# Kernel tuning notes

Measured on AMD Instinct MI355X. Metric: run time of the kernel, lower is better.

The kernel has to match this reference:

```python
import jax, jax.numpy as jnp
import numpy as np

B, T, D, HD, HN, O = 32, 512, 512, 64, 16, 512
EPS = 1e-5


def setup_inputs() -> dict:
    key = jax.random.key(0)
    ks = jax.random.split(key, 12)
    s = lambda fan_in: 1.0 / np.sqrt(fan_in)
    inp = {
        "inputs": jax.random.normal(ks[0], (B, T, D), dtype=jnp.float32),
        "Wq": jax.random.uniform(ks[1], (HN, D, HD), jnp.float32, -s(D), s(D)),
        "bq": jnp.zeros((HN, HD), jnp.float32),
        "Wk": jax.random.uniform(ks[2], (HN, D, HD), jnp.float32, -s(D), s(D)),
        "bk": jnp.zeros((HN, HD), jnp.float32),
        "Wv": jax.random.uniform(ks[3], (HN, D, HD), jnp.float32, -s(D), s(D)),
        "bv": jnp.zeros((HN, HD), jnp.float32),
        "Wr": jax.random.uniform(ks[4], (D, O), jnp.float32, -s(D), s(D)),
        "br": jnp.zeros((O,), jnp.float32),
        "Wo": jax.random.uniform(ks[5], (HN * HD, O), jnp.float32, -s(HN * HD), s(HN * HD)),
        "bo": jnp.zeros((O,), jnp.float32),
        "ln1_w": jnp.ones((O,), jnp.float32),
        "ln1_b": jnp.zeros((O,), jnp.float32),
        "Wfc": jax.random.uniform(ks[6], (O, O), jnp.float32, -s(O), s(O)),
        "bfc": jnp.zeros((O,), jnp.float32),
        "ln2_w": jnp.ones((O,), jnp.float32),
        "ln2_b": jnp.zeros((O,), jnp.float32),
    }
    return inp


def _layernorm(x, w, b):
    mu = jnp.mean(x, axis=-1, keepdims=True)
    var = jnp.mean(jnp.square(x - mu), axis=-1, keepdims=True)
    return (x - mu) * jax.lax.rsqrt(var + EPS) * w + b


def reference(inputs, Wq, bq, Wk, bk, Wv, bv, Wr, br, Wo, bo,
              ln1_w, ln1_b, Wfc, bfc, ln2_w, ln2_b):
    # causal mask: multiply-then-subtract as in the original
    score_mask = jnp.tril(jnp.ones((T, T), jnp.float32))        # [T,T]
    padding_mask = (score_mask == 0).astype(jnp.float32) * 1e9  # [T,T]

    residual = inputs @ Wr + br                                  # [B,T,O]

    # batched per-head projections with nonstandard activations
    q = jax.nn.relu(jnp.einsum('btd,hdf->bhtf', inputs, Wq) + bq[None, :, None, :])
    k = jax.nn.relu(jnp.einsum('btd,hdf->bhtf', inputs, Wk) + bk[None, :, None, :])
    v = jnp.tanh(jnp.einsum('btd,hdf->bhtf', inputs, Wv) + bv[None, :, None, :])

    scores = jnp.einsum('bhtf,bhsf->bhts', q, k) / jnp.sqrt(jnp.float32(HD))
    scores = scores * score_mask - padding_mask                  # [B,H,T,T]
    weights = jax.nn.softmax(scores, axis=-1)
    heads = jnp.einsum('bhts,bhsf->bhtf', weights, v)            # [B,H,T,HD]

    # concat heads (head order preserved) + tanh output projection
    concat = heads.transpose(0, 2, 1, 3).reshape(B, T, HN * HD)
    out = jnp.tanh(concat @ Wo + bo)                             # [B,T,O]

    out = _layernorm(out + residual, ln1_w, ln1_b)
    fc = jax.nn.relu(out @ Wfc + bfc)
    out = _layernorm(fc + out, ln2_w, ln2_b)
    return out
```

## Files before the change

### kernel.cpp

```cpp
#include <hip/hip_runtime.h>
#include <hip/hip_bf16.h>

#define B_  32
#define T_  512
#define D_  512
#define HD_ 64
#define HN_ 16
#define O_  512
#define M_  (B_ * T_)
#define NQ_ (HN_ * HD_)

typedef __bf16 bf16;
typedef __attribute__((ext_vector_type(8))) __bf16 bf16x8;
typedef __attribute__((ext_vector_type(4))) __bf16 bf16x4;
typedef __attribute__((ext_vector_type(4))) float f32x4;

static __device__ __forceinline__ f32x4 mfma16(bf16x8 a, bf16x8 b, f32x4 c) {
    return __builtin_amdgcn_mfma_f32_16x16x32_bf16(a, b, c, 0, 0, 0);
}

static __device__ __forceinline__ void load_lds_16B(const bf16* g, bf16* l) {
    __builtin_amdgcn_global_load_lds(
        (const __attribute__((address_space(1))) unsigned int*)(unsigned long long)g,
        (__attribute__((address_space(3))) unsigned int*)(unsigned long long)l,
        16, 0, 0);
}

static __device__ __forceinline__ float fast_tanh(float x) {
    return 1.f - 2.f / (__expf(2.f * x) + 1.f);
}

static __device__ __forceinline__ int2 swz_block() {
    const int nx = gridDim.x;
    const int nwg = nx * gridDim.y;
    int l = blockIdx.y * nx + blockIdx.x;
    l = (l & 7) * (nwg >> 3) + (l >> 3);
    return make_int2(l % nx, l / nx);
}

__global__ __launch_bounds__(256) void prep_all_kernel(
    const float* __restrict__ inputs,
    const float* __restrict__ Wq, const float* __restrict__ Wk,
    const float* __restrict__ Wv, const float* __restrict__ Wr,
    const float* __restrict__ Wo, const float* __restrict__ Wfc,
    const float* __restrict__ bq, const float* __restrict__ bk,
    const float* __restrict__ bv, const float* __restrict__ br,
    bf16* __restrict__ xin, bf16* __restrict__ wall,
    bf16* __restrict__ wrt, bf16* __restrict__ wot, bf16* __restrict__ wfct,
    float* __restrict__ ball)
{
    __shared__ bf16 tl[64][72];
    const int tid = threadIdx.x;
    int id = blockIdx.x;

    if (id < 4096) {
        const size_t i = ((size_t)id * 256 + tid) * 8;
        f32x4 x0 = *(const f32x4*)(inputs + i);
        f32x4 x1 = *(const f32x4*)(inputs + i + 4);
        bf16x8 v;
        v[0] = (bf16)x0[0]; v[1] = (bf16)x0[1]; v[2] = (bf16)x0[2]; v[3] = (bf16)x0[3];
        v[4] = (bf16)x1[0]; v[5] = (bf16)x1[1]; v[6] = (bf16)x1[2]; v[7] = (bf16)x1[3];
        *(bf16x8*)(xin + i) = v;
        return;
    }
    if (id < 4480) {
        id -= 4096;
        const int kt = id & 7; id >>= 3;
        const int h = id & 15; id >>= 4;
        const float* src = (id == 0) ? Wq : (id == 1) ? Wk : Wv;
        bf16* dst = wall + (size_t)id * (1024 * 512);
        const int k0 = kt * 64;
#pragma unroll
        for (int i = 0; i < 4; i++) {
            const int e = i * 256 + tid;
            const int kk = e >> 4, f4 = (e & 15) * 4;
            const f32x4 v = *(const f32x4*)(src + ((size_t)h * 512 + k0 + kk) * 64 + f4);
#pragma unroll
            for (int j = 0; j < 4; j++) tl[f4 + j][kk] = (bf16)v[j];
        }
        __syncthreads();
#pragma unroll
        for (int i = 0; i < 2; i++) {
            const int e = i * 256 + tid;
            const int f = e >> 3, kc = (e & 7) * 8;
            *(bf16x8*)(dst + ((size_t)h * 64 + f) * 512 + k0 + kc) = *(const bf16x8*)&tl[f][kc];
        }
        return;
    }
    if (id < 4736) {
        id -= 4480;
        const float* src; bf16* dst; int K;
        if (id < 64)       { src = Wr;  dst = wrt;  K = 512;  }
        else if (id < 192) { src = Wo;  dst = wot;  K = 1024; id -= 64; }
        else               { src = Wfc; dst = wfct; K = 512;  id -= 192; }
        const int kt = id >> 3, nt = id & 7;
        const int k0 = kt * 64, n0 = nt * 64;
#pragma unroll
        for (int i = 0; i < 4; i++) {
            const int e = i * 256 + tid;
            const int kk = e >> 4, n4 = (e & 15) * 4;
            const f32x4 v = *(const f32x4*)(src + (size_t)(k0 + kk) * 512 + n0 + n4);
#pragma unroll
            for (int j = 0; j < 4; j++) tl[n4 + j][kk] = (bf16)v[j];
        }
        __syncthreads();
#pragma unroll
        for (int i = 0; i < 2; i++) {
            const int e = i * 256 + tid;
            const int nn = e >> 3, kc = (e & 7) * 8;
            *(bf16x8*)(dst + (size_t)(n0 + nn) * K + k0 + kc) = *(const bf16x8*)&tl[nn][kc];
        }
        return;
    }
    const int i = (id - 4736) * 256 + tid;
    float v = (i < 1024) ? bq[i]
            : (i < 2048) ? bk[i - 1024]
            : (i < 3072) ? bv[i - 2048] : br[i - 3072];
    ball[i] = v;
}

__global__ __launch_bounds__(512, 2) void gemm_qkvr256_kernel(
    const bf16* __restrict__ A, const bf16* __restrict__ Wall,
    const float* __restrict__ ball,
    bf16* __restrict__ qc, bf16* __restrict__ kb, bf16* __restrict__ vt,
    bf16* __restrict__ resb)
{
    __shared__ bf16 SL[65536];
    const int tid = threadIdx.x;
    const int lane = tid & 63;
    const int w = tid >> 6;
    const int wm = w >> 2, wn = w & 3;
    const int lr = lane & 15, lg = lane >> 4;
    const int K = 512;

    const int2 bc = swz_block();
    const int m0 = bc.y * 256, n0 = bc.x * 256;

    const int srow = tid >> 2;
    const int g0 = (tid & 3) ^ ((srow >> 1) & 3);
    const bf16* aP = A + (size_t)(m0 + srow) * K + g0 * 8;
    const bf16* bP = Wall + (size_t)(n0 + srow) * K + g0 * 8;

    auto STAGE = [&](int t) {
        bf16* Ab = SL + (t & 3) * 8192;
        bf16* Bb = SL + 32768 + (t & 3) * 8192;
        const int k0 = t << 5;
        load_lds_16B(aP + k0, Ab + tid * 8);
        load_lds_16B(aP + k0 + (size_t)128 * K, Ab + (512 + tid) * 8);
        load_lds_16B(bP + k0, Bb + tid * 8);
        load_lds_16B(bP + k0 + (size_t)128 * K, Bb + (512 + tid) * 8);
    };

    f32x4 acc[8][4];
    const f32x4 zero4 = {0.f, 0.f, 0.f, 0.f};
#pragma unroll
    for (int i = 0; i < 8; i++)
#pragma unroll
        for (int j = 0; j < 4; j++) acc[i][j] = zero4;

    STAGE(0); STAGE(1); STAGE(2);

    for (int t = 0; t < 16; t++) {
        if (t <= 13)      asm volatile("s_waitcnt vmcnt(8)" ::: "memory");
        else if (t == 14) asm volatile("s_waitcnt vmcnt(4)" ::: "memory");
        else              asm volatile("s_waitcnt vmcnt(0)" ::: "memory");
        asm volatile("s_barrier" ::: "memory");

        const bf16* Ab = SL + (t & 3) * 8192;
        const bf16* Bb = SL + 32768 + (t & 3) * 8192;

        bf16x8 bfr[4], afr[4];
#pragma unroll
        for (int nj = 0; nj < 4; nj++) {
            const int row = wn * 64 + nj * 16 + lr;
            bfr[nj] = *(const bf16x8*)&Bb[row * 32 + ((lg ^ ((row >> 1) & 3)) << 3)];
        }
#pragma unroll
        for (int mi = 0; mi < 4; mi++) {
            const int row = wm * 128 + mi * 16 + lr;
            afr[mi] = *(const bf16x8*)&Ab[row * 32 + ((lg ^ ((row >> 1) & 3)) << 3)];
        }
        if (t <= 12) STAGE(t + 3);
        __builtin_amdgcn_s_setprio(1);
#pragma unroll
        for (int mi = 0; mi < 4; mi++)
#pragma unroll
            for (int nj = 0; nj < 4; nj++)
                acc[mi][nj] = mfma16(afr[mi], bfr[nj], acc[mi][nj]);
        __builtin_amdgcn_s_setprio(0);
        asm volatile("s_barrier" ::: "memory");

#pragma unroll
        for (int mi = 0; mi < 4; mi++) {
            const int row = wm * 128 + (mi + 4) * 16 + lr;
            afr[mi] = *(const bf16x8*)&Ab[row * 32 + ((lg ^ ((row >> 1) & 3)) << 3)];
        }
        __builtin_amdgcn_s_setprio(1);
#pragma unroll
        for (int mi = 0; mi < 4; mi++)
#pragma unroll
            for (int nj = 0; nj < 4; nj++)
                acc[mi + 4][nj] = mfma16(afr[mi], bfr[nj], acc[mi + 4][nj]);
        __builtin_amdgcn_s_setprio(0);
    }
    __syncthreads();

    const int region = n0 >> 10;
    if (region == 2) {
#pragma unroll
        for (int mi = 0; mi < 8; mi++) {
#pragma unroll
            for (int nj = 0; nj < 4; nj++) {
                const int n = n0 + wn * 64 + nj * 16 + lr;
                const float bn = ball[n];
                const int m = m0 + wm * 128 + mi * 16 + lg * 4;
                const int bb = m >> 9, tt = m & 511;
                const int nn = n - 2048, hh = nn >> 6, f = nn & 63;
                bf16x4 st;
#pragma unroll
                for (int r = 0; r < 4; r++) st[r] = (bf16)fast_tanh(acc[mi][nj][r] + bn);
                *(bf16x4*)(vt + (((size_t)(bb * 16 + hh) * 64 + f) << 9) + tt) = st;
            }
        }
    } else {
        bf16* dst; int pitch, nb; float scale = 1.f; bool rl = false;
        if (region == 0)      { dst = qc;   pitch = 1024; nb = n0;        scale = 0.125f; rl = true; }
        else if (region == 1) { dst = kb;   pitch = 1024; nb = n0 - 1024; rl = true; }
        else                  { dst = resb; pitch = 512;  nb = n0 - 3072; }
        float bn[4];
#pragma unroll
        for (int nj = 0; nj < 4; nj++) bn[nj] = ball[n0 + wn * 64 + nj * 16 + lr];
#pragma unroll
        for (int half = 0; half < 2; half++) {
            if (wm == half) {
#pragma unroll
                for (int mi = 0; mi < 8; mi++) {
#pragma unroll
                    for (int nj = 0; nj < 4; nj++) {
                        const int col = wn * 64 + nj * 16 + lr;
#pragma unroll
                        for (int r = 0; r < 4; r++) {
                            float v = acc[mi][nj][r] + bn[nj];
                            if (rl) v = fmaxf(v, 0.f);
                            SL[(mi * 16 + lg * 4 + r) * 264 + col] = (bf16)(v * scale);
                        }
                    }
                }
            }
            __syncthreads();
#pragma unroll
            for (int i = 0; i < 4; i++) {
                const int rr = i * 32 + (tid >> 4);
                const int cc = (tid & 15) * 16;
                bf16x8 v0 = *(const bf16x8*)&SL[rr * 264 + cc];
                bf16x8 v1 = *(const bf16x8*)&SL[rr * 264 + cc + 8];
                bf16* p = dst + (size_t)(m0 + half * 128 + rr) * pitch + nb + cc;
                *(bf16x8*)p = v0;
                *(bf16x8*)(p + 8) = v1;
            }
            __syncthreads();
        }
    }
}

__device__ __forceinline__ void gemm_mainloop_p4(
    const bf16* __restrict__ A, const bf16* __restrict__ Wt,
    const int K, const int m0, const int n0, const int tid,
    bf16* SL, f32x4 (&acc)[4][4])
{
    const int lane = tid & 63;
    const int w = tid >> 6;
    const int wr = w >> 1, wc = w & 1;
    const int lr = lane & 15, lg = lane >> 4;
    const int nt = K >> 5;

    const int r0 = tid >> 2, s0 = tid & 3;
    const int g0 = s0 ^ ((r0 >> 1) & 3);
    const int r1 = r0 + 64;
    const int g1 = s0 ^ ((r1 >> 1) & 3);
    const bf16* aS0 = A + (size_t)(m0 + r0) * K + g0 * 8;
    const bf16* aS1 = A + (size_t)(m0 + r1) * K + g1 * 8;
    const bf16* bS0 = Wt + (size_t)(n0 + r0) * K + g0 * 8;
    const bf16* bS1 = Wt + (size_t)(n0 + r1) * K + g1 * 8;

    auto STAGE = [&](int t) {
        bf16* Ab = SL + (t & 3) * 4096;
        bf16* Bb = SL + 16384 + (t & 3) * 4096;
        const int k0 = t << 5;
        load_lds_16B(aS0 + k0, Ab + tid * 8);
        load_lds_16B(aS1 + k0, Ab + (tid + 256) * 8);
        load_lds_16B(bS0 + k0, Bb + tid * 8);
        load_lds_16B(bS1 + k0, Bb + (tid + 256) * 8);
    };

    STAGE(0); STAGE(1);
    asm volatile("s_waitcnt vmcnt(4)" ::: "memory");
    __builtin_amdgcn_s_barrier();

    for (int t = 0; t < nt; t++) {
        if (t + 2 < nt) {
            STAGE(t + 2);
            asm volatile("s_waitcnt vmcnt(4)" ::: "memory");
        } else {
            asm volatile("s_waitcnt vmcnt(0)" ::: "memory");
        }
        __builtin_amdgcn_s_barrier();

        const bf16* Ab = SL + (t & 3) * 4096;
        const bf16* Bb = SL + 16384 + (t & 3) * 4096;
        bf16x8 a[4], b[4];
#pragma unroll
        for (int mi = 0; mi < 4; mi++) {
            const int row = wr * 64 + mi * 16 + lr;
            a[mi] = *(const bf16x8*)&Ab[row * 32 + ((lg ^ ((row >> 1) & 3)) << 3)];
        }
#pragma unroll
        for (int nj = 0; nj < 4; nj++) {
            const int row = wc * 64 + nj * 16 + lr;
            b[nj] = *(const bf16x8*)&Bb[row * 32 + ((lg ^ ((row >> 1) & 3)) << 3)];
        }
        __builtin_amdgcn_s_setprio(1);
#pragma unroll
        for (int mi = 0; mi < 4; mi++)
#pragma unroll
            for (int nj = 0; nj < 4; nj++)
                acc[mi][nj] = mfma16(a[mi], b[nj], acc[mi][nj]);
        __builtin_amdgcn_s_setprio(0);
    }
    __builtin_amdgcn_s_barrier();
}

template <int ACT>
__global__ __launch_bounds__(256) void gemm_std_kernel(
    const bf16* __restrict__ A, const bf16* __restrict__ Wt,
    const float* __restrict__ bias, bf16* __restrict__ C, const int K)
{
    __shared__ bf16 SL[32768];
    const int tid = threadIdx.x;
    const int2 bc = swz_block();
    const int m0 = bc.y * 128, n0 = bc.x * 128;
    f32x4 acc[4][4];
    const f32x4 zero4 = {0.f, 0.f, 0.f, 0.f};
#pragma unroll
    for (int i = 0; i < 4; i++)
#pragma unroll
        for (int j = 0; j < 4; j++) acc[i][j] = zero4;

    gemm_mainloop_p4(A, Wt, K, m0, n0, tid, SL, acc);

    const int lane = tid & 63, w = tid >> 6;
    const int wr = w >> 1, wc = w & 1, lr = lane & 15, lg = lane >> 4;
#pragma unroll
    for (int mi = 0; mi < 4; mi++) {
#pragma unroll
        for (int nj = 0; nj < 4; nj++) {
            const float bn = bias[n0 + wc * 64 + nj * 16 + lr];
            const int rbase = wr * 64 + mi * 16 + lg * 4;
            const int cidx = wc * 64 + nj * 16 + lr;
#pragma unroll
            for (int r = 0; r < 4; r++) {
                float v = acc[mi][nj][r] + bn;
                if constexpr (ACT == 1) v = fmaxf(v, 0.f);
                else if constexpr (ACT == 2) v = fast_tanh(v);
                SL[(rbase + r) * 136 + cidx] = (bf16)v;
            }
        }
    }
    __syncthreads();
#pragma unroll
    for (int pass = 0; pass < 4; pass++) {
        const int rr = pass * 32 + (tid >> 3);
        const int cc = (tid & 7) * 16;
        bf16x8 v0 = *(const bf16x8*)&SL[rr * 136 + cc];
        bf16x8 v1 = *(const bf16x8*)&SL[rr * 136 + cc + 8];
        *(bf16x8*)(C + (size_t)(m0 + rr) * 512 + n0 + cc) = v0;
        *(bf16x8*)(C + (size_t)(m0 + rr) * 512 + n0 + cc + 8) = v1;
    }
}

static __device__ __forceinline__ int sigma_k(int t) {
    return (t & 32) | ((t & 4) << 2) | ((t & 24) >> 1) | (t & 3);
}

__global__ __launch_bounds__(256) void mfma_attn_kernel(
    const bf16* __restrict__ Kb, const bf16* __restrict__ Vt, bf16* __restrict__ QC)
{
    __shared__ bf16 Ks[2][64][72];
    __shared__ bf16 Vts[2][64][72];

    int l = blockIdx.x;
    l = (l & 7) * 256 + (l >> 3);
    const int qb = l & 3;
    const int h = (l >> 2) & 15;
    const int b = l >> 6;
    const int tid = threadIdx.x;
    const int lane = tid & 63;
    const int w = tid >> 6;
    const int lr = lane & 15, lg = lane >> 4;

    const int qrow0 = qb * 128 + w * 32;
    const size_t qbase = ((size_t)b * T_ + qrow0) * NQ_ + h * 64;
    const int bh = b * HN_ + h;

    bf16x8 qf[2][2];
#pragma unroll
    for (int mi = 0; mi < 2; mi++)
#pragma unroll
        for (int kc = 0; kc < 2; kc++)
            qf[mi][kc] = *(const bf16x8*)(QC + qbase + (size_t)(mi * 16 + lr) * NQ_ + kc * 32 + lg * 8);

    const f32x4 zero4 = {0.f, 0.f, 0.f, 0.f};
    f32x4 o[2][4];
    float m_st[2] = {-1e30f, -1e30f}, l_st[2] = {0.f, 0.f};
#pragma unroll
    for (int mi = 0; mi < 2; mi++)
#pragma unroll
        for (int dj = 0; dj < 4; dj++) o[mi][dj] = zero4;

    const int nsb = 2 * qb + 2;

    bf16x8 kreg[2], vreg[2];
    auto LOADR = [&](int sb) {
#pragma unroll
        for (int i = 0; i < 2; i++) {
            const int ci = i * 256 + tid, row = ci >> 3, cc = ci & 7;
            kreg[i] = *(const bf16x8*)(Kb + ((size_t)b * T_ + sb * 64 + row) * NQ_ + h * 64 + cc * 8);
            vreg[i] = *(const bf16x8*)(Vt + ((size_t)bh * 64 + row) * T_ + sb * 64 + cc * 8);
        }
    };
    auto WRITE = [&](int buf) {
#pragma unroll
        for (int i = 0; i < 2; i++) {
            const int ci = i * 256 + tid, row = ci >> 3, cc = ci & 7;
            *(bf16x8*)&Ks[buf][sigma_k(row)][cc * 8] = kreg[i];
            *(bf16x8*)&Vts[buf][row][cc * 8] = vreg[i];
        }
    };

    LOADR(0); WRITE(0); __syncthreads();
    int cur = 0;

    for (int sb = 0; sb < nsb; sb++) {
        const bool pf = (sb + 1 < nsb);
        if (pf) LOADR(sb + 1);

        if (sb * 64 <= qrow0 + 31) {
            f32x4 sc[2][4];
#pragma unroll
            for (int mi = 0; mi < 2; mi++)
#pragma unroll
                for (int nj = 0; nj < 4; nj++) sc[mi][nj] = zero4;
            __builtin_amdgcn_s_setprio(1);
#pragma unroll
            for (int kc = 0; kc < 2; kc++) {
                bf16x8 kf[4];
#pragma unroll
                for (int nj = 0; nj < 4; nj++)
                    kf[nj] = *(const bf16x8*)&Ks[cur][nj * 16 + lr][kc * 32 + lg * 8];
#pragma unroll
                for (int mi = 0; mi < 2; mi++)
#pragma unroll
                    for (int nj = 0; nj < 4; nj++)
                        sc[mi][nj] = mfma16(kf[nj], qf[mi][kc], sc[mi][nj]);
            }
            __builtin_amdgcn_s_setprio(0);
            const bool needmask = (sb * 64 + 63 > qrow0);
            float tm[2];
#pragma unroll
            for (int mi = 0; mi < 2; mi++) {
                const int qg = qrow0 + mi * 16 + lr;
                float mx = -1e30f;
#pragma unroll
                for (int nj = 0; nj < 4; nj++) {
                    const int kvb = sb * 64 + ((nj >> 1) << 5) + ((nj & 1) << 2) + lg * 8;
#pragma unroll
                    for (int r = 0; r < 4; r++) {
                        float s = sc[mi][nj][r];
                        if (needmask && (kvb + r > qg)) s = -1e30f;
                        sc[mi][nj][r] = s;
                        mx = fmaxf(mx, s);
                    }
                }
                mx = fmaxf(mx, __shfl_xor(mx, 16));
                mx = fmaxf(mx, __shfl_xor(mx, 32));
                tm[mi] = mx;
            }
            const bool defer = (tm[0] <= m_st[0] + 8.f) && (tm[1] <= m_st[1] + 8.f);
            if (!__all(defer)) {
#pragma unroll
                for (int mi = 0; mi < 2; mi++) {
                    const float mn = fmaxf(m_st[mi], tm[mi]);
                    const float sf = __expf(m_st[mi] - mn);
                    m_st[mi] = mn;
                    l_st[mi] *= sf;
#pragma unroll
                    for (int dj = 0; dj < 4; dj++)
#pragma unroll
                        for (int r = 0; r < 4; r++) o[mi][dj][r] *= sf;
                }
            }
            bf16x4 pk[2][4];
#pragma unroll
            for (int mi = 0; mi < 2; mi++) {
                float ts = 0.f;
#pragma unroll
                for (int nj = 0; nj < 4; nj++)
#pragma unroll
                    for (int r = 0; r < 4; r++) {
                        const float p = __expf(sc[mi][nj][r] - m_st[mi]);
                        ts += p;
                        pk[mi][nj][r] = (bf16)p;
                    }
                ts += __shfl_xor(ts, 16);
                ts += __shfl_xor(ts, 32);
                l_st[mi] += ts;
            }
            __builtin_amdgcn_s_setprio(1);
#pragma unroll
            for (int kc = 0; kc < 2; kc++) {
                bf16x8 vf[4], pf2[2];
#pragma unroll
                for (int mi = 0; mi < 2; mi++) {
                    bf16x8 t;
#pragma unroll
                    for (int r = 0; r < 4; r++) { t[r] = pk[mi][2 * kc][r]; t[r + 4] = pk[mi][2 * kc + 1][r]; }
                    pf2[mi] = t;
                }
#pragma unroll
                for (int dj = 0; dj < 4; dj++)
                    vf[dj] = *(const bf16x8*)&Vts[cur][dj * 16 + lr][kc * 32 + lg * 8];
#pragma unroll
                for (int mi = 0; mi < 2; mi++)
#pragma unroll
                    for (int dj = 0; dj < 4; dj++)
                        o[mi][dj] = mfma16(vf[dj], pf2[mi], o[mi][dj]);
            }
            __builtin_amdgcn_s_setprio(0);
        }

        if (pf) WRITE(cur ^ 1);
        __syncthreads();
        cur ^= 1;
    }

#pragma unroll
    for (int mi = 0; mi < 2; mi++) {
        const float inv = 1.f / l_st[mi];
        const size_t rowoff = qbase + (size_t)(mi * 16 + lr) * NQ_;
#pragma unroll
        for (int dj = 0; dj < 4; dj++) {
            bf16x4 st;
#pragma unroll
            for (int r = 0; r < 4; r++) st[r] = (bf16)(o[mi][dj][r] * inv);
            *(bf16x4*)(QC + rowoff + dj * 16 + lg * 4) = st;
        }
    }
}

template <bool F32OUT>
__global__ __launch_bounds__(256) void ln_kernel(
    const bf16* __restrict__ xa, const bf16* __restrict__ xb,
    const float* __restrict__ w, const float* __restrict__ bias,
    void* __restrict__ outv)
{
    const int row = blockIdx.x * 4 + (threadIdx.x >> 6);
    const int ln = threadIdx.x & 63;
    const size_t base = (size_t)row * 512 + ln * 8;
    const bf16x8 va = *(const bf16x8*)(xa + base);
    const bf16x8 vb = *(const bf16x8*)(xb + base);
    float x[8];
    float s = 0.f;
#pragma unroll
    for (int i = 0; i < 8; i++) { x[i] = (float)va[i] + (float)vb[i]; s += x[i]; }
#pragma unroll
    for (int off = 32; off >= 1; off >>= 1) s += __shfl_xor(s, off);
    const float mean = s * (1.f / 512.f);
    float ss = 0.f;
#pragma unroll
    for (int i = 0; i < 8; i++) { x[i] -= mean; ss += x[i] * x[i]; }
#pragma unroll
    for (int off = 32; off >= 1; off >>= 1) ss += __shfl_xor(ss, off);
    const float inv = rsqrtf(ss * (1.f / 512.f) + 1e-5f);
    const f32x4 w0 = *(const f32x4*)(w + ln * 8);
    const f32x4 w1 = *(const f32x4*)(w + ln * 8 + 4);
    const f32x4 b0 = *(const f32x4*)(bias + ln * 8);
    const f32x4 b1 = *(const f32x4*)(bias + ln * 8 + 4);
    if constexpr (F32OUT) {
        f32x4 y0, y1;
#pragma unroll
        for (int i = 0; i < 4; i++) {
            y0[i] = x[i] * inv * w0[i] + b0[i];
            y1[i] = x[4 + i] * inv * w1[i] + b1[i];
        }
        *(f32x4*)((float*)outv + base) = y0;
        *(f32x4*)((float*)outv + base + 4) = y1;
    } else {
        bf16x8 y;
#pragma unroll
        for (int i = 0; i < 4; i++) {
            y[i] = (bf16)(x[i] * inv * w0[i] + b0[i]);
            y[4 + i] = (bf16)(x[4 + i] * inv * w1[i] + b1[i]);
        }
        *(bf16x8*)((bf16*)outv + base) = y;
    }
}

extern "C" void kernel_launch(void* const* d_in, const int* in_sizes, int n_in,
                              void* d_out, int out_size, void* d_ws, size_t ws_size,
                              hipStream_t stream)
{
    const float* inputs = (const float*)d_in[0];
    const float* Wq = (const float*)d_in[1];
    const float* bq = (const float*)d_in[2];
    const float* Wk = (const float*)d_in[3];
    const float* bk = (const float*)d_in[4];
    const float* Wv = (const float*)d_in[5];
    const float* bv = (const float*)d_in[6];
    const float* Wr = (const float*)d_in[7];
    const float* br = (const float*)d_in[8];
    const float* Wo = (const float*)d_in[9];
    const float* bo = (const float*)d_in[10];
    const float* ln1w = (const float*)d_in[11];
    const float* ln1b = (const float*)d_in[12];
    const float* Wfc = (const float*)d_in[13];
    const float* bfc = (const float*)d_in[14];
    const float* ln2w = (const float*)d_in[15];
    const float* ln2b = (const float*)d_in[16];
    float* out = (float*)d_out;

    const size_t MB = 1024ull * 1024ull;
    char* ws = (char*)d_ws;
    bf16* qc   = (bf16*)(ws);
    bf16* kb   = (bf16*)(ws + 32 * MB);
    bf16* vt   = (bf16*)(ws + 64 * MB);
    bf16* xin  = (bf16*)(ws + 96 * MB);
    bf16* wall = (bf16*)(ws + 112 * MB);
    bf16* wot  = (bf16*)(ws + 112 * MB + 3670016);
    bf16* wfct = (bf16*)(ws + 112 * MB + 3670016 + 1048576);
    float* ball = (float*)(ws + 112 * MB + 3670016 + 1048576 + 524288);
    bf16* wrt  = wall + (size_t)3072 * 512;
    bf16* resb = (bf16*)d_out;
    bf16* att  = kb;
    bf16* ln1  = kb + (size_t)8 * MB;
    bf16* fcb  = vt;

    const dim3 blk(256);

    prep_all_kernel<<<dim3(4750), blk, 0, stream>>>(
        inputs, Wq, Wk, Wv, Wr, Wo, Wfc, bq, bk, bv, br,
        xin, wall, wrt, wot, wfct, ball);

    gemm_qkvr256_kernel<<<dim3(14, 64), dim3(512), 0, stream>>>(
        xin, wall, ball, qc, kb, vt, resb);
    mfma_attn_kernel<<<dim3(B_ * HN_ * 4), blk, 0, stream>>>(kb, vt, qc);
    gemm_std_kernel<2><<<dim3(4, 128), blk, 0, stream>>>(qc, wot, bo, att, 1024);
    ln_kernel<false><<<dim3(4096), blk, 0, stream>>>(att, resb, ln1w, ln1b, ln1);
    gemm_std_kernel<1><<<dim3(4, 128), blk, 0, stream>>>(ln1, wfct, bfc, fcb, 512);
    ln_kernel<true ><<<dim3(4096), blk, 0, stream>>>(fcb, ln1, ln2w, ln2b, out);
}
```

Measured before the change: 251.5 us.

## Restructure QKVR GEMM mainloop to 64-wide K tiles with quarter-stage double buffering

The QKVR projection GEMM mainloop moves from a 4-deep ring of 32-wide K tiles to a 2-slot double buffer of 64-wide K tiles. Each tile's global-to-LDS copy is split into four quarter-stages, issued between the four MFMA sub-blocks so loads for the next tile overlap compute at finer grain. The change halves the number of K iterations and uses a new 8-way XOR swizzle for the wider rows, aiming to cut barrier and wait overhead per MFMA. In exchange it adds more barriers inside each iteration and leaves less prefetch depth, so memory stalls could become visible. Some variables are renamed to avoid shadowing.

```diff
diff --git a/kernel.cpp b/kernel.cpp
--- a/kernel.cpp
+++ b/kernel.cpp
@@ -136,19 +136,41 @@
     const int2 bc = swz_block();
     const int m0 = bc.y * 256, n0 = bc.x * 256;
 
-    const int srow = tid >> 2;
-    const int g0 = (tid & 3) ^ ((srow >> 1) & 3);
-    const bf16* aP = A + (size_t)(m0 + srow) * K + g0 * 8;
-    const bf16* bP = Wall + (size_t)(n0 + srow) * K + g0 * 8;
-
-    auto STAGE = [&](int t) {
-        bf16* Ab = SL + (t & 3) * 8192;
-        bf16* Bb = SL + 32768 + (t & 3) * 8192;
-        const int k0 = t << 5;
-        load_lds_16B(aP + k0, Ab + tid * 8);
-        load_lds_16B(aP + k0 + (size_t)128 * K, Ab + (512 + tid) * 8);
-        load_lds_16B(bP + k0, Bb + tid * 8);
-        load_lds_16B(bP + k0 + (size_t)128 * K, Bb + (512 + tid) * 8);
+    const int p = tid & 7;
+    const int rr = tid >> 3;
+    const int g = p ^ (rr & 7);
+    const int arow0 = rr, arow1 = 128 + rr;
+    const int brow0 = ((rr >> 5) << 6) | (rr & 31);
+    const int brow1 = 128 + brow0;
+
+    auto STAGE_H = [&](int t, int h) {
+        const int slot = t & 1;
+        const int k0 = t << 6;
+        if ((h & 1) == 0) {
+            bf16* Bb = SL + 32768 + slot * 16384;
+            const int off = (h == 2) ? 32 : 0;
+            const int r0_ = brow0 + off, r1_ = brow1 + off;
+            load_lds_16B(Wall + (size_t)(n0 + r0_) * K + k0 + g * 8, Bb + r0_ * 64 + p * 8);
+            load_lds_16B(Wall + (size_t)(n0 + r1_) * K + k0 + g * 8, Bb + r1_ * 64 + p * 8);
+        } else {
+            bf16* Ab = SL + slot * 16384;
+            const int off = (h == 3) ? 64 : 0;
+            const int r0_ = arow0 + off, r1_ = arow1 + off;
+            load_lds_16B(A + (size_t)(m0 + r0_) * K + k0 + g * 8, Ab + r0_ * 64 + p * 8);
+            load_lds_16B(A + (size_t)(m0 + r1_) * K + k0 + g * 8, Ab + r1_ * 64 + p * 8);
+        }
+    };
+
+    const int x = lr & 7;
+    auto LDA = [&](int t, int mi, int kc) -> bf16x8 {
+        const int row = wm * 128 + mi * 16 + lr;
+        const bf16* Ab = SL + (t & 1) * 16384;
+        return *(const bf16x8*)&Ab[row * 64 + ((((kc << 2) | lg) ^ x) << 3)];
+    };
+    auto LDB = [&](int t, int nj, int kc) -> bf16x8 {
+        const int row = wn * 64 + nj * 16 + lr;
+        const bf16* Bb = SL + 32768 + (t & 1) * 16384;
+        return *(const bf16x8*)&Bb[row * 64 + ((((kc << 2) | lg) ^ x) << 3)];
     };
 
     f32x4 acc[8][4];
@@ -158,49 +180,126 @@
 #pragma unroll
         for (int j = 0; j < 4; j++) acc[i][j] = zero4;
 
-    STAGE(0); STAGE(1); STAGE(2);
-
-    for (int t = 0; t < 16; t++) {
-        if (t <= 13)      asm volatile("s_waitcnt vmcnt(8)" ::: "memory");
-        else if (t == 14) asm volatile("s_waitcnt vmcnt(4)" ::: "memory");
-        else              asm volatile("s_waitcnt vmcnt(0)" ::: "memory");
-        asm volatile("s_barrier" ::: "memory");
-
-        const bf16* Ab = SL + (t & 3) * 8192;
-        const bf16* Bb = SL + 32768 + (t & 3) * 8192;
-
-        bf16x8 bfr[4], afr[4];
-#pragma unroll
-        for (int nj = 0; nj < 4; nj++) {
-            const int row = wn * 64 + nj * 16 + lr;
-            bfr[nj] = *(const bf16x8*)&Bb[row * 32 + ((lg ^ ((row >> 1) & 3)) << 3)];
-        }
-#pragma unroll
-        for (int mi = 0; mi < 4; mi++) {
-            const int row = wm * 128 + mi * 16 + lr;
-            afr[mi] = *(const bf16x8*)&Ab[row * 32 + ((lg ^ ((row >> 1) & 3)) << 3)];
-        }
-        if (t <= 12) STAGE(t + 3);
+    bf16x8 b01[4], b23[4], af[8];
+
+    STAGE_H(0, 0); STAGE_H(0, 1); STAGE_H(0, 2); STAGE_H(0, 3);
+
+    for (int t = 0; t < 7; t++) {
+        asm volatile("s_waitcnt vmcnt(4)\n\ts_barrier" ::: "memory");
+#pragma unroll
+        for (int nj = 0; nj < 2; nj++)
+#pragma unroll
+            for (int kc = 0; kc < 2; kc++) b01[nj * 2 + kc] = LDB(t, nj, kc);
+#pragma unroll
+        for (int mi = 0; mi < 4; mi++)
+#pragma unroll
+            for (int kc = 0; kc < 2; kc++) af[mi * 2 + kc] = LDA(t, mi, kc);
+        STAGE_H(t + 1, 0);
         __builtin_amdgcn_s_setprio(1);
 #pragma unroll
         for (int mi = 0; mi < 4; mi++)
 #pragma unroll
-            for (int nj = 0; nj < 4; nj++)
-                acc[mi][nj] = mfma16(afr[mi], bfr[nj], acc[mi][nj]);
+            for (int nj = 0; nj < 2; nj++)
+#pragma unroll
+                for (int kc = 0; kc < 2; kc++)
+                    acc[mi][nj] = mfma16(af[mi * 2 + kc], b01[nj * 2 + kc], acc[mi][nj]);
         __builtin_amdgcn_s_setprio(0);
-        asm volatile("s_barrier" ::: "memory");
-
-#pragma unroll
-        for (int mi = 0; mi < 4; mi++) {
-            const int row = wm * 128 + (mi + 4) * 16 + lr;
-            afr[mi] = *(const bf16x8*)&Ab[row * 32 + ((lg ^ ((row >> 1) & 3)) << 3)];
-        }
+        asm volatile("s_waitcnt vmcnt(4)\n\ts_barrier" ::: "memory");
+#pragma unroll
+        for (int nj = 0; nj < 2; nj++)
+#pragma unroll
+            for (int kc = 0; kc < 2; kc++) b23[nj * 2 + kc] = LDB(t, nj + 2, kc);
+        STAGE_H(t + 1, 1);
         __builtin_amdgcn_s_setprio(1);
 #pragma unroll
         for (int mi = 0; mi < 4; mi++)
 #pragma unroll
-            for (int nj = 0; nj < 4; nj++)
-                acc[mi + 4][nj] = mfma16(afr[mi], bfr[nj], acc[mi + 4][nj]);
+            for (int nj = 0; nj < 2; nj++)
+#pragma unroll
+                for (int kc = 0; kc < 2; kc++)
+                    acc[mi][nj + 2] = mfma16(af[mi * 2 + kc], b23[nj * 2 + kc], acc[mi][nj + 2]);
+        __builtin_amdgcn_s_setprio(0);
+        asm volatile("s_waitcnt vmcnt(4)\n\ts_barrier" ::: "memory");
+#pragma unroll
+        for (int mi = 0; mi < 4; mi++)
+#pragma unroll
+            for (int kc = 0; kc < 2; kc++) af[mi * 2 + kc] = LDA(t, mi + 4, kc);
+        STAGE_H(t + 1, 2);
+        __builtin_amdgcn_s_setprio(1);
+#pragma unroll
+        for (int mi = 0; mi < 4; mi++)
+#pragma unroll
+            for (int nj = 0; nj < 2; nj++)
+#pragma unroll
+                for (int kc = 0; kc < 2; kc++)
+                    acc[mi + 4][nj] = mfma16(af[mi * 2 + kc], b01[nj * 2 + kc], acc[mi + 4][nj]);
+        __builtin_amdgcn_s_setprio(0);
+        STAGE_H(t + 1, 3);
+        __builtin_amdgcn_s_setprio(1);
+#pragma unroll
+        for (int mi = 0; mi < 4; mi++)
+#pragma unroll
+            for (int nj = 0; nj < 2; nj++)
+#pragma unroll
+                for (int kc = 0; kc < 2; kc++)
+                    acc[mi + 4][nj + 2] = mfma16(af[mi * 2 + kc], b23[nj * 2 + kc], acc[mi + 4][nj + 2]);
+        __builtin_amdgcn_s_setprio(0);
+    }
+
+    {
+        const int t = 7;
+        asm volatile("s_waitcnt vmcnt(4)\n\ts_barrier" ::: "memory");
+#pragma unroll
+        for (int nj = 0; nj < 2; nj++)
+#pragma unroll
+            for (int kc = 0; kc < 2; kc++) b01[nj * 2 + kc] = LDB(t, nj, kc);
+#pragma unroll
+        for (int mi = 0; mi < 4; mi++)
+#pragma unroll
+            for (int kc = 0; kc < 2; kc++) af[mi * 2 + kc] = LDA(t, mi, kc);
+        __builtin_amdgcn_s_setprio(1);
+#pragma unroll
+        for (int mi = 0; mi < 4; mi++)
+#pragma unroll
+            for (int nj = 0; nj < 2; nj++)
+#pragma unroll
+                for (int kc = 0; kc < 2; kc++)
+                    acc[mi][nj] = mfma16(af[mi * 2 + kc], b01[nj * 2 + kc], acc[mi][nj]);
+        __builtin_amdgcn_s_setprio(0);
+        asm volatile("s_waitcnt vmcnt(2)\n\ts_barrier" ::: "memory");
+#pragma unroll
+        for (int nj = 0; nj < 2; nj++)
+#pragma unroll
+            for (int kc = 0; kc < 2; kc++) b23[nj * 2 + kc] = LDB(t, nj + 2, kc);
+        __builtin_amdgcn_s_setprio(1);
+#pragma unroll
+        for (int mi = 0; mi < 4; mi++)
+#pragma unroll
+            for (int nj = 0; nj < 2; nj++)
+#pragma unroll
+                for (int kc = 0; kc < 2; kc++)
+                    acc[mi][nj + 2] = mfma16(af[mi * 2 + kc], b23[nj * 2 + kc], acc[mi][nj + 2]);
+        __builtin_amdgcn_s_setprio(0);
+        asm volatile("s_waitcnt vmcnt(0)\n\ts_barrier" ::: "memory");
+#pragma unroll
+        for (int mi = 0; mi < 4; mi++)
+#pragma unroll
+            for (int kc = 0; kc < 2; kc++) af[mi * 2 + kc] = LDA(t, mi + 4, kc);
+        __builtin_amdgcn_s_setprio(1);
+#pragma unroll
+        for (int mi = 0; mi < 4; mi++)
+#pragma unroll
+            for (int nj = 0; nj < 2; nj++)
+#pragma unroll
+                for (int kc = 0; kc < 2; kc++)
+                    acc[mi + 4][nj] = mfma16(af[mi * 2 + kc], b01[nj * 2 + kc], acc[mi + 4][nj]);
+#pragma unroll
+        for (int mi = 0; mi < 4; mi++)
+#pragma unroll
+            for (int nj = 0; nj < 2; nj++)
+#pragma unroll
+                for (int kc = 0; kc < 2; kc++)
+                    acc[mi + 4][nj + 2] = mfma16(af[mi * 2 + kc], b23[nj * 2 + kc], acc[mi + 4][nj + 2]);
         __builtin_amdgcn_s_setprio(0);
     }
     __syncthreads();
@@ -250,13 +349,13 @@
             __syncthreads();
 #pragma unroll
             for (int i = 0; i < 4; i++) {
-                const int rr = i * 32 + (tid >> 4);
+                const int rr2 = i * 32 + (tid >> 4);
                 const int cc = (tid & 15) * 16;
-                bf16x8 v0 = *(const bf16x8*)&SL[rr * 264 + cc];
-                bf16x8 v1 = *(const bf16x8*)&SL[rr * 264 + cc + 8];
-                bf16* p = dst + (size_t)(m0 + half * 128 + rr) * pitch + nb + cc;
-                *(bf16x8*)p = v0;
-                *(bf16x8*)(p + 8) = v1;
+                bf16x8 v0 = *(const bf16x8*)&SL[rr2 * 264 + cc];
+                bf16x8 v1 = *(const bf16x8*)&SL[rr2 * 264 + cc + 8];
+                bf16* pdst = dst + (size_t)(m0 + half * 128 + rr2) * pitch + nb + cc;
+                *(bf16x8*)pdst = v0;
+                *(bf16x8*)(pdst + 8) = v1;
             }
             __syncthreads();
         }
@@ -507,9 +606,9 @@
                 for (int nj = 0; nj < 4; nj++)
 #pragma unroll
                     for (int r = 0; r < 4; r++) {
-                        const float p = __expf(sc[mi][nj][r] - m_st[mi]);
-                        ts += p;
-                        pk[mi][nj][r] = (bf16)p;
+                        const float p2 = __expf(sc[mi][nj][r] - m_st[mi]);
+                        ts += p2;
+                        pk[mi][nj][r] = (bf16)p2;
                     }
                 ts += __shfl_xor(ts, 16);
                 ts += __shfl_xor(ts, 32);
```

Measured after the change: 244.7 us. -2.7%, faster.
